# Optimization experiments

Measured on AMD Instinct MI355X. Metric: run time of the kernel, lower is better.

## Reference

```python
import jax, jax.numpy as jnp
import numpy as np

N_NODES = 100000
N_EDGES = 600000
D_IN = 128
D_OUT = 128
N_REL = 16
N_BASES = 8


def setup_inputs() -> dict:
    key = jax.random.key(0)
    ks = jax.random.split(key, 6)
    x = jax.random.normal(ks[0], (N_NODES, D_IN), dtype=jnp.float32)
    edge_index = jax.random.randint(ks[1], (2, N_EDGES), 0, N_NODES, dtype=jnp.int64)
    edge_type = jax.random.randint(ks[2], (N_EDGES,), 0, N_REL, dtype=jnp.int64)
    # xavier-uniform-ish init scales
    b_lim = float(np.sqrt(6.0 / (D_IN + D_OUT)))
    c_lim = float(np.sqrt(6.0 / (N_REL + N_BASES)))
    w_lim = float(np.sqrt(6.0 / (D_IN + D_OUT)))
    bases = jax.random.uniform(ks[3], (N_BASES, D_IN, D_OUT), jnp.float32, -b_lim, b_lim)
    coefficients = jax.random.uniform(ks[4], (N_REL, N_BASES), jnp.float32, -c_lim, c_lim)
    w_self = jax.random.uniform(ks[5], (D_OUT, D_IN), jnp.float32, -w_lim, w_lim)
    return {"x": x, "edge_index": edge_index, "edge_type": edge_type,
            "bases": bases, "coefficients": coefficients, "w_self": w_self}


def reference(x, edge_index, edge_type, bases, coefficients, w_self):
    # self loop: Linear(in, out, bias=False) -> x @ W^T
    out = x @ w_self.T  # [N, D_OUT]
    # relation weights from basis decomposition
    weights = jnp.einsum('rb,bio->rio', coefficients, bases)  # [R, D_IN, D_OUT]
    row, col = edge_index[0], edge_index[1]
    xc = x[col]  # [E, D_IN] gather of source features
    n_rel = weights.shape[0]
    msg = jnp.zeros((xc.shape[0], w_self.shape[0]), dtype=x.dtype)
    # fixed small loop over relations; masked accumulate matches per-relation grouped GEMM
    for r in range(n_rel):
        sel = (edge_type == r)[:, None]
        msg = msg + jnp.where(sel, xc @ weights[r], jnp.zeros((), x.dtype))
    # scatter-add messages to destination rows
    out = out.at[row].add(msg)
    return out
```

## Files before the change

kernel.cpp:

```cpp
#include <hip/hip_runtime.h>

#define NN 100000
#define NE 600000
#define ET (NE + NN)
#define D 128
#define NREL 16
#define SCANB 391
#define TPB 4
#define MAXTILES 10954
#define GEMMG ((MAXTILES + TPB - 1) / TPB)
#define WGRID 1088

typedef short short8 __attribute__((ext_vector_type(8)));
typedef float f32x4 __attribute__((ext_vector_type(4)));
typedef unsigned int u32x4 __attribute__((ext_vector_type(4)));

#define C0 0
#define O0 20
#define CU0 40
#define T0 60

#define WT_OFF   0
#define META_OFF 557056
#define DH_OFF   557568
#define DO_OFF   957568
#define DC_OFF   1357576
#define BS_OFF   1757576
#define SCP_OFF  1759576
#define SR_OFF   7360088
#define XB_OFF   10160096
#define MSGB_OFF 35760096
#define MSGA_OFF 10160096
#define NEED_B   (MSGB_OFF + (size_t)ET * 128 * 2)
#define NEED_A   (MSGA_OFF + (size_t)ET * 128 * 2)

__device__ __forceinline__ unsigned short f2bf(float f) {
  unsigned u = __builtin_bit_cast(unsigned, f);
  u += 0x7fffu + ((u >> 16) & 1u);
  return (unsigned short)(u >> 16);
}

__global__ __launch_bounds__(256) void k_prep(const float* __restrict__ bases,
    const float* __restrict__ coef, const float* __restrict__ w_self,
    unsigned short* __restrict__ wT, const float* __restrict__ x,
    unsigned short* __restrict__ xb)
{
  if (blockIdx.x < WGRID) {
    int idx = blockIdx.x * 256 + threadIdx.x;
    int r = idx >> 14;
    int t = idx & 16383;
    float v;
    if (r < 16) {
      int o = t >> 7, i = t & 127;
      float acc = 0.f;
      #pragma unroll
      for (int b = 0; b < 8; ++b)
        acc += coef[r * 8 + b] * bases[b * 16384 + i * 128 + o];
      v = acc;
    } else {
      v = w_self[t];
    }
    wT[idx] = f2bf(v);
  } else {
    int i = (blockIdx.x - WGRID) * 256 + threadIdx.x;
    if (i >= NN * D / 4) return;
    float4 f = *(const float4*)(x + (size_t)i * 4);
    unsigned short s0 = f2bf(f.x), s1 = f2bf(f.y), s2 = f2bf(f.z), s3 = f2bf(f.w);
    unsigned long long pk = (unsigned long long)s0 | ((unsigned long long)s1 << 16)
                          | ((unsigned long long)s2 << 32) | ((unsigned long long)s3 << 48);
    *(unsigned long long*)(xb + (size_t)i * 4) = pk;
  }
}

__global__ __launch_bounds__(256) void k_hist(const int* __restrict__ ei,
    const int* __restrict__ et, int* __restrict__ meta, int* __restrict__ dstHist)
{
  __shared__ int h[16];
  int tid = threadIdx.x;
  if (tid < 16) h[tid] = 0;
  __syncthreads();
  for (int e = blockIdx.x * 256 + tid; e < NE; e += gridDim.x * 256) {
    atomicAdd(&h[et[e]], 1);
    atomicAdd(&dstHist[ei[e]], 1);
  }
  __syncthreads();
  if (tid < 16) atomicAdd(&meta[C0 + tid], h[tid]);
}

__global__ __launch_bounds__(256) void k_scan1(const int* __restrict__ dstHist,
    int* __restrict__ dstOff, int* __restrict__ blockSums)
{
  __shared__ int sh[256];
  int tid = threadIdx.x;
  int d = blockIdx.x * 256 + tid;
  int v = (d < NN) ? (dstHist[d] + 1) : 0;
  sh[tid] = v;
  __syncthreads();
  #pragma unroll
  for (int ofs = 1; ofs < 256; ofs <<= 1) {
    int t = (tid >= ofs) ? sh[tid - ofs] : 0;
    __syncthreads();
    sh[tid] += t;
    __syncthreads();
  }
  if (d < NN) dstOff[d] = sh[tid] - v;
  if (tid == 255) blockSums[blockIdx.x] = sh[tid];
}

__global__ __launch_bounds__(512) void k_scan2(int* __restrict__ blockSums, int* __restrict__ meta)
{
  __shared__ int sh[SCANB];
  int tid = threadIdx.x;
  if (tid < SCANB) sh[tid] = blockSums[tid];
  __syncthreads();
  if (tid == 0) {
    int run = 0;
    for (int i = 0; i < SCANB; ++i) { int c = sh[i]; sh[i] = run; run += c; }
    meta[C0 + 16] = NN;
    int off = 0, toff = 0;
    for (int r = 0; r <= 16; ++r) {
      meta[O0 + r] = off;
      meta[CU0 + r] = off;
      meta[T0 + r] = toff;
      int c = meta[C0 + r];
      off += c;
      toff += (c + 63) >> 6;
    }
    meta[O0 + 17] = off;
    meta[T0 + 17] = toff;
  }
  __syncthreads();
  if (tid < SCANB) blockSums[tid] = sh[tid];
}

__global__ __launch_bounds__(256) void k_scan3(int* __restrict__ dstOff,
    const int* __restrict__ blockSums, int* __restrict__ dstCursor,
    int2* __restrict__ sCP)
{
  int tid = threadIdx.x;
  int d = blockIdx.x * 256 + tid;
  int base = blockSums[blockIdx.x];
  if (d < NN) {
    int o = dstOff[d] + base;
    dstOff[d] = o;
    dstCursor[d] = o + 1;
    sCP[NE + d] = make_int2(d, o);
  }
  if (d == NN) dstOff[NN] = ET;
}

__global__ __launch_bounds__(256) void k_self0(int2* __restrict__ sCP, int* __restrict__ sRow)
{
  int n = blockIdx.x * 256 + threadIdx.x;
  if (n < NN) { sCP[NE + n] = make_int2(n, 0); sRow[NE + n] = n; }
}

__global__ __launch_bounds__(256) void k_scatter(const int* __restrict__ ei, const int* __restrict__ et,
    int* __restrict__ meta, int2* __restrict__ sCP, int* __restrict__ sRow,
    int* __restrict__ dstCursor, int doMsg)
{
  __shared__ int h[16], base[16], lh[16];
  int tid = threadIdx.x;
  int start = blockIdx.x * 4096;
  int end = min(NE, start + 4096);
  if (tid < 16) { h[tid] = 0; lh[tid] = 0; }
  __syncthreads();
  for (int e = start + tid; e < end; e += 256)
    atomicAdd(&h[et[e]], 1);
  __syncthreads();
  if (tid < 16) base[tid] = atomicAdd(&meta[CU0 + tid], h[tid]);
  __syncthreads();
  for (int e = start + tid; e < end; e += 256) {
    int r = et[e];
    int row = ei[e];
    int pos = base[r] + atomicAdd(&lh[r], 1);
    int slot = doMsg ? atomicAdd(&dstCursor[row], 1) : 0;
    sCP[pos] = make_int2(ei[NE + e], slot);
    if (!doMsg) sRow[pos] = row;
  }
}

__global__ __launch_bounds__(256) void k_gemm(const float* __restrict__ xf,
    const unsigned short* __restrict__ xb,
    const unsigned short* __restrict__ wT, const int* __restrict__ meta,
    const int2* __restrict__ sCP, const int* __restrict__ sRow,
    unsigned short* __restrict__ msg, float* __restrict__ out,
    int xbf, int msgmode)
{
  __shared__ short As[64 * 17 * 8];
  __shared__ short Es[64 * 136];
  __shared__ int Pos2[2][64];
  __shared__ int Rows[64];
  __shared__ int Ms[80];

  int tid = threadIdx.x;
  if (tid < 80) Ms[tid] = meta[tid];
  __syncthreads();
  int ntiles = Ms[T0 + 17];

  int lane = tid & 63, wave = tid >> 6;
  int q = lane >> 4, l15 = lane & 15;
  int m = tid >> 2, ug = tid & 3;

  if (xbf && msgmode) {
    short8 pf[4];
    int pcy = 0;
    bool pvalid = false;
    int r = 0, nr = 0;
    int b = blockIdx.x * TPB;
    if (b < ntiles) {
      while (r < 16 && Ms[T0 + r + 1] <= b) ++r;
      int boff = Ms[O0 + r];
      int e0 = boff + (b - Ms[T0 + r]) * 64;
      nr = min(64, boff + Ms[C0 + r] - e0);
      pvalid = m < nr;
      int2 cp = sCP[pvalid ? (e0 + m) : e0];
      pcy = cp.y;
      const unsigned short* xr = xb + (size_t)cp.x * 128;
      #pragma unroll
      for (int s = 0; s < 4; ++s) {
        short8 v = (short8)(short)0;
        if (pvalid) v = *(const short8*)(xr + (ug * 4 + s) * 8);
        pf[s] = v;
      }
    }
    int rprev = -1;
    short8 bfr[2][4];
    for (int ti = 0; ti < TPB; ++ti) {
      b = blockIdx.x * TPB + ti;
      if (b >= ntiles) break;
      int curR = r, curNr = nr;
      #pragma unroll
      for (int s = 0; s < 4; ++s)
        *(short8*)&As[(m * 17 + ug * 4 + s) * 8] = pf[s];
      if (ug == 0) Pos2[ti & 1][m] = pvalid ? pcy : 0;
      __syncthreads();
      int bn = b + 1;
      if (ti + 1 < TPB && bn < ntiles) {
        int rn = curR;
        while (rn < 16 && Ms[T0 + rn + 1] <= bn) ++rn;
        int boff = Ms[O0 + rn];
        int e0n = boff + (bn - Ms[T0 + rn]) * 64;
        int nrn = min(64, boff + Ms[C0 + rn] - e0n);
        pvalid = m < nrn;
        int2 cp = sCP[pvalid ? (e0n + m) : e0n];
        pcy = cp.y;
        const unsigned short* xr = xb + (size_t)cp.x * 128;
        #pragma unroll
        for (int s = 0; s < 4; ++s) {
          short8 v = (short8)(short)0;
          if (pvalid) v = *(const short8*)(xr + (ug * 4 + s) * 8);
          pf[s] = v;
        }
        r = rn; nr = nrn;
      }
      if (curR != rprev) {
        const unsigned short* wr = wT + curR * 16384;
        #pragma unroll
        for (int ns = 0; ns < 2; ++ns)
          #pragma unroll
          for (int kk = 0; kk < 4; ++kk)
            bfr[ns][kk] = *(const short8*)(wr + (wave * 32 + ns * 16 + l15) * 128 + kk * 32 + q * 8);
        rprev = curR;
      }
      f32x4 acc[4][2];
      #pragma unroll
      for (int ms = 0; ms < 4; ++ms)
        #pragma unroll
        for (int ns = 0; ns < 2; ++ns)
          acc[ms][ns] = (f32x4){0.f, 0.f, 0.f, 0.f};
      #pragma unroll
      for (int kk = 0; kk < 4; ++kk) {
        short8 af[4];
        #pragma unroll
        for (int ms = 0; ms < 4; ++ms)
          af[ms] = *(const short8*)&As[((ms * 16 + l15) * 17 + kk * 4 + q) * 8];
        #pragma unroll
        for (int ms = 0; ms < 4; ++ms)
          #pragma unroll
          for (int ns = 0; ns < 2; ++ns)
            acc[ms][ns] = __builtin_amdgcn_mfma_f32_16x16x32_bf16(af[ms], bfr[ns][kk], acc[ms][ns], 0, 0, 0);
      }
      #pragma unroll
      for (int ms = 0; ms < 4; ++ms)
        #pragma unroll
        for (int ns = 0; ns < 2; ++ns)
          #pragma unroll
          for (int reg = 0; reg < 4; ++reg)
            Es[(ms * 16 + q * 4 + reg) * 136 + wave * 32 + ns * 16 + l15] =
                (short)f2bf(acc[ms][ns][reg]);
      __syncthreads();
      #pragma unroll
      for (int i = 0; i < 4; ++i) {
        int row = wave * 16 + i * 4 + q;
        short8 v = *(const short8*)&Es[row * 136 + l15 * 8];
        if (row < curNr)
          *(short8*)(msg + (size_t)Pos2[ti & 1][row] * 128 + l15 * 8) = v;
      }
    }
    return;
  }

  int rprev = -1;
  short8 bfr[2][4];
  for (int ti = 0; ti < TPB; ++ti) {
    int b = blockIdx.x * TPB + ti;
    if (b >= ntiles) break;
    int r = 0;
    while (r < 16 && Ms[T0 + r + 1] <= b) ++r;
    int tile = b - Ms[T0 + r];
    int boff = Ms[O0 + r];
    int e0 = boff + tile * 64;
    int nrows = min(64, boff + Ms[C0 + r] - e0);

    bool valid = m < nrows;
    int e = valid ? (e0 + m) : e0;
    int2 cp = sCP[e];
    if (ug == 0) {
      Pos2[0][m] = valid ? cp.y : 0;
      if (!msgmode) Rows[m] = valid ? sRow[e] : 0;
    }
    int c = cp.x;
    if (xbf) {
      const unsigned short* xr = xb + (size_t)c * 128;
      #pragma unroll
      for (int s = 0; s < 4; ++s) {
        int u = ug * 4 + s;
        short8 pk = (short8)(short)0;
        if (valid) pk = *(const short8*)(xr + u * 8);
        *(short8*)&As[(m * 17 + u) * 8] = pk;
      }
    } else {
      const float* xr = xf + (size_t)c * 128;
      #pragma unroll
      for (int s = 0; s < 4; ++s) {
        int u = ug * 4 + s;
        float4 f0 = make_float4(0.f, 0.f, 0.f, 0.f), f1 = f0;
        if (valid) {
          f0 = *(const float4*)(xr + u * 8);
          f1 = *(const float4*)(xr + u * 8 + 4);
        }
        short8 pk;
        pk[0] = (short)f2bf(f0.x); pk[1] = (short)f2bf(f0.y);
        pk[2] = (short)f2bf(f0.z); pk[3] = (short)f2bf(f0.w);
        pk[4] = (short)f2bf(f1.x); pk[5] = (short)f2bf(f1.y);
        pk[6] = (short)f2bf(f1.z); pk[7] = (short)f2bf(f1.w);
        *(short8*)&As[(m * 17 + u) * 8] = pk;
      }
    }
    __syncthreads();

    if (r != rprev) {
      const unsigned short* wr = wT + r * 16384;
      #pragma unroll
      for (int ns = 0; ns < 2; ++ns)
        #pragma unroll
        for (int kk = 0; kk < 4; ++kk)
          bfr[ns][kk] = *(const short8*)(wr + (wave * 32 + ns * 16 + l15) * 128 + kk * 32 + q * 8);
      rprev = r;
    }

    f32x4 acc[4][2];
    #pragma unroll
    for (int ms = 0; ms < 4; ++ms)
      #pragma unroll
      for (int ns = 0; ns < 2; ++ns)
        acc[ms][ns] = (f32x4){0.f, 0.f, 0.f, 0.f};
    #pragma unroll
    for (int kk = 0; kk < 4; ++kk) {
      short8 af[4];
      #pragma unroll
      for (int ms = 0; ms < 4; ++ms)
        af[ms] = *(const short8*)&As[((ms * 16 + l15) * 17 + kk * 4 + q) * 8];
      #pragma unroll
      for (int ms = 0; ms < 4; ++ms)
        #pragma unroll
        for (int ns = 0; ns < 2; ++ns)
          acc[ms][ns] = __builtin_amdgcn_mfma_f32_16x16x32_bf16(af[ms], bfr[ns][kk], acc[ms][ns], 0, 0, 0);
    }

    if (msgmode) {
      __syncthreads();
      #pragma unroll
      for (int ms = 0; ms < 4; ++ms)
        #pragma unroll
        for (int ns = 0; ns < 2; ++ns)
          #pragma unroll
          for (int reg = 0; reg < 4; ++reg)
            Es[(ms * 16 + q * 4 + reg) * 136 + wave * 32 + ns * 16 + l15] =
                (short)f2bf(acc[ms][ns][reg]);
      __syncthreads();
      #pragma unroll
      for (int i = 0; i < 4; ++i) {
        int row = wave * 16 + i * 4 + q;
        short8 v = *(const short8*)&Es[row * 136 + l15 * 8];
        if (row < nrows)
          *(short8*)(msg + (size_t)Pos2[0][row] * 128 + l15 * 8) = v;
      }
      __syncthreads();
    } else {
      #pragma unroll
      for (int ms = 0; ms < 4; ++ms)
        #pragma unroll
        for (int reg = 0; reg < 4; ++reg) {
          int mrow = ms * 16 + q * 4 + reg;
          if (mrow < nrows) {
            float* op = out + (size_t)Rows[mrow] * 128 + wave * 32 + l15;
            unsafeAtomicAdd(op, acc[ms][0][reg]);
            unsafeAtomicAdd(op + 16, acc[ms][1][reg]);
          }
        }
      __syncthreads();
    }
  }
}

__global__ __launch_bounds__(256) void k_reduce(const unsigned short* __restrict__ msg,
    const int* __restrict__ dstOff, float* __restrict__ out)
{
  int d = blockIdx.x * 16 + (threadIdx.x >> 4);
  if (d >= NN) return;
  int sl = threadIdx.x & 15;
  int s = dstOff[d], e = dstOff[d + 1];
  const unsigned short* base = msg + (size_t)sl * 8;
  float a[8], bacc[8];
  #pragma unroll
  for (int i = 0; i < 8; ++i) { a[i] = 0.f; bacc[i] = 0.f; }
  int j = s;
  for (; j + 1 < e; j += 2) {
    u32x4 v0 = *(const u32x4*)(base + (size_t)j * 128);
    u32x4 v1 = *(const u32x4*)(base + (size_t)(j + 1) * 128);
    #pragma unroll
    for (int c = 0; c < 4; ++c) {
      a[2 * c]     += __builtin_bit_cast(float, v0[c] << 16);
      a[2 * c + 1] += __builtin_bit_cast(float, v0[c] & 0xffff0000u);
      bacc[2 * c]     += __builtin_bit_cast(float, v1[c] << 16);
      bacc[2 * c + 1] += __builtin_bit_cast(float, v1[c] & 0xffff0000u);
    }
  }
  if (j < e) {
    u32x4 v0 = *(const u32x4*)(base + (size_t)j * 128);
    #pragma unroll
    for (int c = 0; c < 4; ++c) {
      a[2 * c]     += __builtin_bit_cast(float, v0[c] << 16);
      a[2 * c + 1] += __builtin_bit_cast(float, v0[c] & 0xffff0000u);
    }
  }
  float4 w0, w1;
  w0.x = a[0] + bacc[0]; w0.y = a[1] + bacc[1]; w0.z = a[2] + bacc[2]; w0.w = a[3] + bacc[3];
  w1.x = a[4] + bacc[4]; w1.y = a[5] + bacc[5]; w1.z = a[6] + bacc[6]; w1.w = a[7] + bacc[7];
  float* op = out + (size_t)d * 128 + sl * 8;
  *(float4*)op = w0;
  *(float4*)(op + 4) = w1;
}

extern "C" void kernel_launch(void* const* d_in, const int* in_sizes, int n_in,
                              void* d_out, int out_size, void* d_ws, size_t ws_size,
                              hipStream_t stream)
{
  const float* x      = (const float*)d_in[0];
  const int*   ei     = (const int*)d_in[1];
  const int*   et     = (const int*)d_in[2];
  const float* bases  = (const float*)d_in[3];
  const float* coef   = (const float*)d_in[4];
  const float* w_self = (const float*)d_in[5];
  float* out = (float*)d_out;
  char* ws = (char*)d_ws;
  unsigned short* wT = (unsigned short*)(ws + WT_OFF);
  int* meta      = (int*)(ws + META_OFF);
  int* dstHist   = (int*)(ws + DH_OFF);
  int* dstOff    = (int*)(ws + DO_OFF);
  int* dstCursor = (int*)(ws + DC_OFF);
  int* blockSums = (int*)(ws + BS_OFF);
  int2* sCP      = (int2*)(ws + SCP_OFF);
  int* sRow      = (int*)(ws + SR_OFF);
  unsigned short* xb = (unsigned short*)(ws + XB_OFF);

  const int modeB = (ws_size >= NEED_B) ? 1 : 0;
  const int modeA = (modeB || ws_size >= NEED_A) ? 1 : 0;
  unsigned short* msg = (unsigned short*)(ws + (modeB ? MSGB_OFF : MSGA_OFF));

  hipMemsetAsync(ws + META_OFF, 0, 512 + 400000, stream);
  k_prep<<<modeB ? (WGRID + 12500) : WGRID, 256, 0, stream>>>(bases, coef, w_self, wT, x, xb);
  k_hist<<<256, 256, 0, stream>>>(ei, et, meta, dstHist);
  if (modeA) {
    k_scan1<<<SCANB, 256, 0, stream>>>(dstHist, dstOff, blockSums);
    k_scan2<<<1, 512, 0, stream>>>(blockSums, meta);
    k_scan3<<<SCANB, 256, 0, stream>>>(dstOff, blockSums, dstCursor, sCP);
  } else {
    k_scan2<<<1, 512, 0, stream>>>(blockSums, meta);
    k_self0<<<SCANB, 256, 0, stream>>>(sCP, sRow);
    hipMemsetAsync(d_out, 0, (size_t)NN * D * 4, stream);
  }
  k_scatter<<<(NE + 4095) / 4096, 256, 0, stream>>>(ei, et, meta, sCP, sRow, dstCursor, modeA);
  k_gemm<<<GEMMG, 256, 0, stream>>>(x, xb, wT, meta, sCP, sRow, msg, out, modeB, modeA);
  if (modeA)
    k_reduce<<<(NN + 15) / 16, 256, 0, stream>>>(msg, dstOff, out);
}
```

Measured before the change: 329.5 us.

## Fuse all pipeline stages into one cooperative persistent kernel with grid syncs

Replaces the chain of separate launches (memset, prep, hist, three scans, scatter, gemm, reduce) with a single cooperative kernel that runs each stage in turn and separates them with grid-wide syncs. This removes per-launch overhead and the gaps between kernels. In exchange, each stage is limited to the occupancy-bounded grid (capped at 2048 blocks). Each grid sync costs time, and the GEMM stage now assigns contiguous tile chunks per block instead of fixed groups of four.

```diff
diff --git a/kernel.cpp b/kernel.cpp
--- a/kernel.cpp
+++ b/kernel.cpp
@@ -1,4 +1,7 @@
 #include <hip/hip_runtime.h>
+#include <hip/hip_cooperative_groups.h>
+
+namespace cg = cooperative_groups;
 
 #define NN 100000
 #define NE 600000
@@ -10,6 +13,8 @@
 #define MAXTILES 10954
 #define GEMMG ((MAXTILES + TPB - 1) / TPB)
 #define WGRID 1088
+#define WTN (17 * 16384)
+#define XCN (NN * D / 4)
 
 typedef short short8 __attribute__((ext_vector_type(8)));
 typedef float f32x4 __attribute__((ext_vector_type(4)));
@@ -40,6 +45,295 @@
   return (unsigned short)(u >> 16);
 }
 
+struct GemmSm {
+  short As[64 * 17 * 8];
+  short Es[64 * 136];
+  int Pos2[2][64];
+  int Ms[80];
+};
+union Sm {
+  GemmSm g;
+  int sh[256];
+  int s2[SCANB];
+  struct { int h[16]; int base[16]; int lh[16]; } sc;
+  int hist[16];
+};
+
+__global__ __launch_bounds__(256) void k_fused(const float* __restrict__ x,
+    const int* __restrict__ ei, const int* __restrict__ et,
+    const float* __restrict__ bases, const float* __restrict__ coef,
+    const float* __restrict__ w_self, unsigned short* __restrict__ wT,
+    int* __restrict__ meta, int* __restrict__ dstHist, int* __restrict__ dstOff,
+    int* __restrict__ dstCursor, int* __restrict__ blockSums,
+    int2* __restrict__ sCP, unsigned short* __restrict__ xb,
+    unsigned short* __restrict__ msg, float* __restrict__ out)
+{
+  cg::grid_group gg = cg::this_grid();
+  __shared__ Sm sm;
+  int tid = threadIdx.x;
+  int gstride = gridDim.x * 256;
+  int gt = blockIdx.x * 256 + tid;
+
+  for (int i = gt; i < NN + 128; i += gstride) {
+    if (i < 128) meta[i] = 0; else dstHist[i - 128] = 0;
+  }
+  gg.sync();
+
+  for (int u = gt; u < WTN + XCN; u += gstride) {
+    if (u < WTN) {
+      int r = u >> 14, t = u & 16383;
+      float v;
+      if (r < 16) {
+        int o = t >> 7, i = t & 127;
+        float acc = 0.f;
+        #pragma unroll
+        for (int b = 0; b < 8; ++b)
+          acc += coef[r * 8 + b] * bases[b * 16384 + i * 128 + o];
+        v = acc;
+      } else {
+        v = w_self[t];
+      }
+      wT[u] = f2bf(v);
+    } else {
+      int i = u - WTN;
+      float4 f = *(const float4*)(x + (size_t)i * 4);
+      unsigned short s0 = f2bf(f.x), s1 = f2bf(f.y), s2v = f2bf(f.z), s3 = f2bf(f.w);
+      unsigned long long pk = (unsigned long long)s0 | ((unsigned long long)s1 << 16)
+                            | ((unsigned long long)s2v << 32) | ((unsigned long long)s3 << 48);
+      *(unsigned long long*)(xb + (size_t)i * 4) = pk;
+    }
+  }
+  __syncthreads();
+  if (tid < 16) sm.hist[tid] = 0;
+  __syncthreads();
+  for (int e = gt; e < NE; e += gstride) {
+    atomicAdd(&sm.hist[et[e]], 1);
+    atomicAdd(&dstHist[ei[e]], 1);
+  }
+  __syncthreads();
+  if (tid < 16) atomicAdd(&meta[C0 + tid], sm.hist[tid]);
+  gg.sync();
+
+  for (int v = blockIdx.x; v < SCANB; v += gridDim.x) {
+    int d = v * 256 + tid;
+    int val = (d < NN) ? (dstHist[d] + 1) : 0;
+    sm.sh[tid] = val;
+    __syncthreads();
+    #pragma unroll
+    for (int ofs = 1; ofs < 256; ofs <<= 1) {
+      int t = (tid >= ofs) ? sm.sh[tid - ofs] : 0;
+      __syncthreads();
+      sm.sh[tid] += t;
+      __syncthreads();
+    }
+    if (d < NN) dstOff[d] = sm.sh[tid] - val;
+    if (tid == 255) blockSums[v] = sm.sh[tid];
+    __syncthreads();
+  }
+  gg.sync();
+
+  if (blockIdx.x == 0) {
+    for (int i = tid; i < SCANB; i += 256) sm.s2[i] = blockSums[i];
+    __syncthreads();
+    if (tid == 0) {
+      int run = 0;
+      for (int i = 0; i < SCANB; ++i) { int c = sm.s2[i]; sm.s2[i] = run; run += c; }
+      meta[C0 + 16] = NN;
+      int off = 0, toff = 0;
+      for (int r = 0; r <= 16; ++r) {
+        meta[O0 + r] = off;
+        meta[CU0 + r] = off;
+        meta[T0 + r] = toff;
+        int c = meta[C0 + r];
+        off += c;
+        toff += (c + 63) >> 6;
+      }
+      meta[O0 + 17] = off;
+      meta[T0 + 17] = toff;
+    }
+    __syncthreads();
+    for (int i = tid; i < SCANB; i += 256) blockSums[i] = sm.s2[i];
+  }
+  gg.sync();
+
+  for (int v = blockIdx.x; v < SCANB; v += gridDim.x) {
+    int d = v * 256 + tid;
+    int base = blockSums[v];
+    if (d < NN) {
+      int o = dstOff[d] + base;
+      dstOff[d] = o;
+      dstCursor[d] = o + 1;
+      sCP[NE + d] = make_int2(d, o);
+    }
+    if (d == NN) dstOff[NN] = ET;
+  }
+  gg.sync();
+
+  for (int v = blockIdx.x; v * 4096 < NE; v += gridDim.x) {
+    int start = v * 4096;
+    int end = min(NE, start + 4096);
+    if (tid < 16) { sm.sc.h[tid] = 0; sm.sc.lh[tid] = 0; }
+    __syncthreads();
+    for (int e = start + tid; e < end; e += 256)
+      atomicAdd(&sm.sc.h[et[e]], 1);
+    __syncthreads();
+    if (tid < 16) sm.sc.base[tid] = atomicAdd(&meta[CU0 + tid], sm.sc.h[tid]);
+    __syncthreads();
+    for (int e = start + tid; e < end; e += 256) {
+      int r = et[e];
+      int row = ei[e];
+      int pos = sm.sc.base[r] + atomicAdd(&sm.sc.lh[r], 1);
+      int slot = atomicAdd(&dstCursor[row], 1);
+      sCP[pos] = make_int2(ei[NE + e], slot);
+    }
+    __syncthreads();
+  }
+  gg.sync();
+
+  if (tid < 80) sm.g.Ms[tid] = meta[tid];
+  __syncthreads();
+  {
+    int ntiles = sm.g.Ms[T0 + 17];
+    int chunk = (ntiles + gridDim.x - 1) / gridDim.x;
+    int t0 = blockIdx.x * chunk;
+    int t1 = min(ntiles, t0 + chunk);
+    int lane = tid & 63, wave = tid >> 6;
+    int q = lane >> 4, l15 = lane & 15;
+    int m = tid >> 2, ug = tid & 3;
+
+    if (t0 < t1) {
+      short8 pf[4];
+      int pcy = 0;
+      bool pvalid = false;
+      int r = 0, nr = 0;
+      {
+        while (r < 16 && sm.g.Ms[T0 + r + 1] <= t0) ++r;
+        int boff = sm.g.Ms[O0 + r];
+        int e0 = boff + (t0 - sm.g.Ms[T0 + r]) * 64;
+        nr = min(64, boff + sm.g.Ms[C0 + r] - e0);
+        pvalid = m < nr;
+        int2 cp = sCP[pvalid ? (e0 + m) : e0];
+        pcy = cp.y;
+        const unsigned short* xr = xb + (size_t)cp.x * 128;
+        #pragma unroll
+        for (int s = 0; s < 4; ++s) {
+          short8 v = (short8)(short)0;
+          if (pvalid) v = *(const short8*)(xr + (ug * 4 + s) * 8);
+          pf[s] = v;
+        }
+      }
+      int rprev = -1;
+      short8 bfr[2][4];
+      for (int b = t0; b < t1; ++b) {
+        int curR = r, curNr = nr;
+        #pragma unroll
+        for (int s = 0; s < 4; ++s)
+          *(short8*)&sm.g.As[(m * 17 + ug * 4 + s) * 8] = pf[s];
+        if (ug == 0) sm.g.Pos2[b & 1][m] = pvalid ? pcy : 0;
+        __syncthreads();
+        int bn = b + 1;
+        if (bn < t1) {
+          int rn = curR;
+          while (rn < 16 && sm.g.Ms[T0 + rn + 1] <= bn) ++rn;
+          int boff = sm.g.Ms[O0 + rn];
+          int e0n = boff + (bn - sm.g.Ms[T0 + rn]) * 64;
+          int nrn = min(64, boff + sm.g.Ms[C0 + rn] - e0n);
+          pvalid = m < nrn;
+          int2 cp = sCP[pvalid ? (e0n + m) : e0n];
+          pcy = cp.y;
+          const unsigned short* xr = xb + (size_t)cp.x * 128;
+          #pragma unroll
+          for (int s = 0; s < 4; ++s) {
+            short8 v = (short8)(short)0;
+            if (pvalid) v = *(const short8*)(xr + (ug * 4 + s) * 8);
+            pf[s] = v;
+          }
+          r = rn; nr = nrn;
+        }
+        if (curR != rprev) {
+          const unsigned short* wr = wT + curR * 16384;
+          #pragma unroll
+          for (int ns = 0; ns < 2; ++ns)
+            #pragma unroll
+            for (int kk = 0; kk < 4; ++kk)
+              bfr[ns][kk] = *(const short8*)(wr + (wave * 32 + ns * 16 + l15) * 128 + kk * 32 + q * 8);
+          rprev = curR;
+        }
+        f32x4 acc[4][2];
+        #pragma unroll
+        for (int ms = 0; ms < 4; ++ms)
+          #pragma unroll
+          for (int ns = 0; ns < 2; ++ns)
+            acc[ms][ns] = (f32x4){0.f, 0.f, 0.f, 0.f};
+        #pragma unroll
+        for (int kk = 0; kk < 4; ++kk) {
+          short8 af[4];
+          #pragma unroll
+          for (int ms = 0; ms < 4; ++ms)
+            af[ms] = *(const short8*)&sm.g.As[((ms * 16 + l15) * 17 + kk * 4 + q) * 8];
+          #pragma unroll
+          for (int ms = 0; ms < 4; ++ms)
+            #pragma unroll
+            for (int ns = 0; ns < 2; ++ns)
+              acc[ms][ns] = __builtin_amdgcn_mfma_f32_16x16x32_bf16(af[ms], bfr[ns][kk], acc[ms][ns], 0, 0, 0);
+        }
+        #pragma unroll
+        for (int ms = 0; ms < 4; ++ms)
+          #pragma unroll
+          for (int ns = 0; ns < 2; ++ns)
+            #pragma unroll
+            for (int reg = 0; reg < 4; ++reg)
+              sm.g.Es[(ms * 16 + q * 4 + reg) * 136 + wave * 32 + ns * 16 + l15] =
+                  (short)f2bf(acc[ms][ns][reg]);
+        __syncthreads();
+        #pragma unroll
+        for (int i = 0; i < 4; ++i) {
+          int row = wave * 16 + i * 4 + q;
+          short8 v = *(const short8*)&sm.g.Es[row * 136 + l15 * 8];
+          if (row < curNr)
+            *(short8*)(msg + (size_t)sm.g.Pos2[b & 1][row] * 128 + l15 * 8) = v;
+        }
+      }
+    }
+  }
+  gg.sync();
+
+  for (int d = blockIdx.x * 16 + (tid >> 4); d < NN; d += gridDim.x * 16) {
+    int sl = tid & 15;
+    int s = dstOff[d], e = dstOff[d + 1];
+    const unsigned short* base = msg + (size_t)sl * 8;
+    float a[8], bacc[8];
+    #pragma unroll
+    for (int i = 0; i < 8; ++i) { a[i] = 0.f; bacc[i] = 0.f; }
+    int j = s;
+    for (; j + 1 < e; j += 2) {
+      u32x4 v0 = *(const u32x4*)(base + (size_t)j * 128);
+      u32x4 v1 = *(const u32x4*)(base + (size_t)(j + 1) * 128);
+      #pragma unroll
+      for (int c = 0; c < 4; ++c) {
+        a[2 * c]     += __builtin_bit_cast(float, v0[c] << 16);
+        a[2 * c + 1] += __builtin_bit_cast(float, v0[c] & 0xffff0000u);
+        bacc[2 * c]     += __builtin_bit_cast(float, v1[c] << 16);
+        bacc[2 * c + 1] += __builtin_bit_cast(float, v1[c] & 0xffff0000u);
+      }
+    }
+    if (j < e) {
+      u32x4 v0 = *(const u32x4*)(base + (size_t)j * 128);
+      #pragma unroll
+      for (int c = 0; c < 4; ++c) {
+        a[2 * c]     += __builtin_bit_cast(float, v0[c] << 16);
+        a[2 * c + 1] += __builtin_bit_cast(float, v0[c] & 0xffff0000u);
+      }
+    }
+    float4 w0, w1;
+    w0.x = a[0] + bacc[0]; w0.y = a[1] + bacc[1]; w0.z = a[2] + bacc[2]; w0.w = a[3] + bacc[3];
+    w1.x = a[4] + bacc[4]; w1.y = a[5] + bacc[5]; w1.z = a[6] + bacc[6]; w1.w = a[7] + bacc[7];
+    float* op = out + (size_t)d * 128 + sl * 8;
+    *(float4*)op = w0;
+    *(float4*)(op + 4) = w1;
+  }
+}
+
 __global__ __launch_bounds__(256) void k_prep(const float* __restrict__ bases,
     const float* __restrict__ coef, const float* __restrict__ w_self,
     unsigned short* __restrict__ wT, const float* __restrict__ x,
@@ -63,7 +357,7 @@
     wT[idx] = f2bf(v);
   } else {
     int i = (blockIdx.x - WGRID) * 256 + threadIdx.x;
-    if (i >= NN * D / 4) return;
+    if (i >= XCN) return;
     float4 f = *(const float4*)(x + (size_t)i * 4);
     unsigned short s0 = f2bf(f.x), s1 = f2bf(f.y), s2 = f2bf(f.z), s3 = f2bf(f.w);
     unsigned long long pk = (unsigned long long)s0 | ((unsigned long long)s1 << 16)
@@ -201,105 +495,6 @@
   int lane = tid & 63, wave = tid >> 6;
   int q = lane >> 4, l15 = lane & 15;
   int m = tid >> 2, ug = tid & 3;
-
-  if (xbf && msgmode) {
-    short8 pf[4];
-    int pcy = 0;
-    bool pvalid = false;
-    int r = 0, nr = 0;
-    int b = blockIdx.x * TPB;
-    if (b < ntiles) {
-      while (r < 16 && Ms[T0 + r + 1] <= b) ++r;
-      int boff = Ms[O0 + r];
-      int e0 = boff + (b - Ms[T0 + r]) * 64;
-      nr = min(64, boff + Ms[C0 + r] - e0);
-      pvalid = m < nr;
-      int2 cp = sCP[pvalid ? (e0 + m) : e0];
-      pcy = cp.y;
-      const unsigned short* xr = xb + (size_t)cp.x * 128;
-      #pragma unroll
-      for (int s = 0; s < 4; ++s) {
-        short8 v = (short8)(short)0;
-        if (pvalid) v = *(const short8*)(xr + (ug * 4 + s) * 8);
-        pf[s] = v;
-      }
-    }
-    int rprev = -1;
-    short8 bfr[2][4];
-    for (int ti = 0; ti < TPB; ++ti) {
-      b = blockIdx.x * TPB + ti;
-      if (b >= ntiles) break;
-      int curR = r, curNr = nr;
-      #pragma unroll
-      for (int s = 0; s < 4; ++s)
-        *(short8*)&As[(m * 17 + ug * 4 + s) * 8] = pf[s];
-      if (ug == 0) Pos2[ti & 1][m] = pvalid ? pcy : 0;
-      __syncthreads();
-      int bn = b + 1;
-      if (ti + 1 < TPB && bn < ntiles) {
-        int rn = curR;
-        while (rn < 16 && Ms[T0 + rn + 1] <= bn) ++rn;
-        int boff = Ms[O0 + rn];
-        int e0n = boff + (bn - Ms[T0 + rn]) * 64;
-        int nrn = min(64, boff + Ms[C0 + rn] - e0n);
-        pvalid = m < nrn;
-        int2 cp = sCP[pvalid ? (e0n + m) : e0n];
-        pcy = cp.y;
-        const unsigned short* xr = xb + (size_t)cp.x * 128;
-        #pragma unroll
-        for (int s = 0; s < 4; ++s) {
-          short8 v = (short8)(short)0;
-          if (pvalid) v = *(const short8*)(xr + (ug * 4 + s) * 8);
-          pf[s] = v;
-        }
-        r = rn; nr = nrn;
-      }
-      if (curR != rprev) {
-        const unsigned short* wr = wT + curR * 16384;
-        #pragma unroll
-        for (int ns = 0; ns < 2; ++ns)
-          #pragma unroll
-          for (int kk = 0; kk < 4; ++kk)
-            bfr[ns][kk] = *(const short8*)(wr + (wave * 32 + ns * 16 + l15) * 128 + kk * 32 + q * 8);
-        rprev = curR;
-      }
-      f32x4 acc[4][2];
-      #pragma unroll
-      for (int ms = 0; ms < 4; ++ms)
-        #pragma unroll
-        for (int ns = 0; ns < 2; ++ns)
-          acc[ms][ns] = (f32x4){0.f, 0.f, 0.f, 0.f};
-      #pragma unroll
-      for (int kk = 0; kk < 4; ++kk) {
-        short8 af[4];
-        #pragma unroll
-        for (int ms = 0; ms < 4; ++ms)
-          af[ms] = *(const short8*)&As[((ms * 16 + l15) * 17 + kk * 4 + q) * 8];
-        #pragma unroll
-        for (int ms = 0; ms < 4; ++ms)
-          #pragma unroll
-          for (int ns = 0; ns < 2; ++ns)
-            acc[ms][ns] = __builtin_amdgcn_mfma_f32_16x16x32_bf16(af[ms], bfr[ns][kk], acc[ms][ns], 0, 0, 0);
-      }
-      #pragma unroll
-      for (int ms = 0; ms < 4; ++ms)
-        #pragma unroll
-        for (int ns = 0; ns < 2; ++ns)
-          #pragma unroll
-          for (int reg = 0; reg < 4; ++reg)
-            Es[(ms * 16 + q * 4 + reg) * 136 + wave * 32 + ns * 16 + l15] =
-                (short)f2bf(acc[ms][ns][reg]);
-      __syncthreads();
-      #pragma unroll
-      for (int i = 0; i < 4; ++i) {
-        int row = wave * 16 + i * 4 + q;
-        short8 v = *(const short8*)&Es[row * 136 + l15 * 8];
-        if (row < curNr)
-          *(short8*)(msg + (size_t)Pos2[ti & 1][row] * 128 + l15 * 8) = v;
-      }
-    }
-    return;
-  }
 
   int rprev = -1;
   short8 bfr[2][4];
@@ -480,6 +675,20 @@
   const int modeA = (modeB || ws_size >= NEED_A) ? 1 : 0;
   unsigned short* msg = (unsigned short*)(ws + (modeB ? MSGB_OFF : MSGA_OFF));
 
+  int occ = 0;
+  hipOccupancyMaxActiveBlocksPerMultiprocessor(&occ, k_fused, 256, 0);
+  int coopGrid = occ * 256;
+  if (coopGrid > 2048) coopGrid = 2048;
+
+  if (modeB && coopGrid >= 256) {
+    void* args[] = { (void*)&x, (void*)&ei, (void*)&et, (void*)&bases, (void*)&coef,
+                     (void*)&w_self, (void*)&wT, (void*)&meta, (void*)&dstHist,
+                     (void*)&dstOff, (void*)&dstCursor, (void*)&blockSums,
+                     (void*)&sCP, (void*)&xb, (void*)&msg, (void*)&out };
+    hipLaunchCooperativeKernel((void*)k_fused, dim3(coopGrid), dim3(256), args, 0, stream);
+    return;
+  }
+
   hipMemsetAsync(ws + META_OFF, 0, 512 + 400000, stream);
   k_prep<<<modeB ? (WGRID + 12500) : WGRID, 256, 0, stream>>>(bases, coef, w_self, wT, x, xb);
   k_hist<<<256, 256, 0, stream>>>(ei, et, meta, dstHist);
```

Result: slower. 603.2 us (+83.1%).
